# Optimization experiments

Hardware: AMD Instinct MI355X
Metric: run time of the kernel (lower is better)

The kernel has to match this reference:

```python
import jax, jax.numpy as jnp
import numpy as np
import math

B, S, D = 4, 1024, 1024
H, DK = 16, 64
NUM_BUCKETS = 32
MAX_DISTANCE = 128


def _relative_position_bucket(relative_position, bidirectional=True,
                              num_buckets=32, max_distance=128):
    # faithful port of T5's bucketing
    relative_buckets = jnp.zeros_like(relative_position)
    if bidirectional:
        num_buckets //= 2
        relative_buckets = relative_buckets + (relative_position > 0).astype(jnp.int32) * num_buckets
        relative_position = jnp.abs(relative_position)
    else:
        relative_position = -jnp.minimum(relative_position, jnp.zeros_like(relative_position))
    max_exact = num_buckets // 2
    is_small = relative_position < max_exact
    rp_safe = jnp.maximum(relative_position, 1)  # avoid log(0); masked by is_small
    rel_if_large = max_exact + (
        jnp.log(rp_safe.astype(jnp.float32) / max_exact)
        / math.log(max_distance / max_exact) * (num_buckets - max_exact)
    ).astype(jnp.int32)
    rel_if_large = jnp.minimum(rel_if_large, num_buckets - 1)
    return relative_buckets + jnp.where(is_small, relative_position, rel_if_large)


def compute_bias(rel_bias_emb, query_length, key_length):
    ctx = jnp.arange(query_length, dtype=jnp.int32)[:, None]
    mem = jnp.arange(key_length, dtype=jnp.int32)[None, :]
    rp = mem - ctx  # [q, k]
    buckets = _relative_position_bucket(rp, bidirectional=True,
                                        num_buckets=NUM_BUCKETS,
                                        max_distance=MAX_DISTANCE)
    values = rel_bias_emb[buckets]          # [q, k, h]
    return jnp.transpose(values, (2, 0, 1))[None]  # [1, h, q, k]


def setup_inputs() -> dict:
    key = jax.random.key(0)
    ks = jax.random.split(key, 6)
    s = 1.0 / math.sqrt(D)
    return {
        "hidden_states": jax.random.normal(ks[0], (B, S, D), jnp.float32),
        "Wq": jax.random.normal(ks[1], (D, H * DK), jnp.float32) * s,
        "Wk": jax.random.normal(ks[2], (D, H * DK), jnp.float32) * s,
        "Wv": jax.random.normal(ks[3], (D, H * DK), jnp.float32) * s,
        "Wo": jax.random.normal(ks[4], (H * DK, D), jnp.float32) * s,
        "rel_bias_emb": jax.random.normal(ks[5], (NUM_BUCKETS, H), jnp.float32),
    }


def reference(hidden_states, Wq, Wk, Wv, Wo, rel_bias_emb):
    b, s, _ = hidden_states.shape

    def shape_heads(x):  # [b, s, h*dk] -> [b, h, s, dk]
        return x.reshape(b, s, H, DK).transpose(0, 2, 1, 3)

    q = shape_heads(hidden_states @ Wq)
    k = shape_heads(hidden_states @ Wk)
    v = shape_heads(hidden_states @ Wv)

    # T5 attention: no 1/sqrt(dk) scaling
    scores = jnp.einsum('bhqd,bhkd->bhqk', q, k)
    position_bias = compute_bias(rel_bias_emb, s, s)  # [1, h, s, s]
    scores = scores + position_bias
    attn = jax.nn.softmax(scores.astype(jnp.float32), axis=-1).astype(scores.dtype)
    ctx = jnp.einsum('bhqk,bhkd->bhqd', attn, v)
    ctx = ctx.transpose(0, 2, 1, 3).reshape(b, s, H * DK)
    return ctx @ Wo
```

## Files before the change

kernel.cpp:

```cpp
#include <hip/hip_runtime.h>

typedef unsigned short u16;
typedef unsigned int u32;
typedef __bf16 bf16x8 __attribute__((ext_vector_type(8)));
typedef float f32x4 __attribute__((ext_vector_type(4)));

#define MFMA16(a, b, c) __builtin_amdgcn_mfma_f32_16x16x32_bf16(a, b, c, 0, 0, 0)
#define LOG2E 1.4426950408889634f

__device__ __forceinline__ u16 f2bf(float f) {
  u32 u = __float_as_uint(f);
  u += 0x7FFFu + ((u >> 16) & 1u);
  return (u16)(u >> 16);
}

__device__ __forceinline__ void gld16(u16* lds, const u16* g) {
  __builtin_amdgcn_global_load_lds((const __attribute__((address_space(1))) void*)g,
                                   (__attribute__((address_space(3))) void*)lds,
                                   16, 0, 0);
}

__device__ __forceinline__ int t5_bucket(int rp) {
  int ret = rp > 0 ? 16 : 0;
  int a = rp < 0 ? -rp : rp;
  int b;
  if      (a <  8) b = a;
  else if (a < 12) b = 8;
  else if (a < 16) b = 9;
  else if (a < 23) b = 10;
  else if (a < 32) b = 11;
  else if (a < 46) b = 12;
  else if (a < 64) b = 13;
  else if (a < 91) b = 14;
  else             b = 15;
  return ret + b;
}

__global__ __launch_bounds__(256) void prep(const float4* __restrict__ X, ushort4* __restrict__ Xb,
                                            const float* __restrict__ w0, const float* __restrict__ w1,
                                            const float* __restrict__ w2, const float* __restrict__ w3,
                                            u16* __restrict__ out) {
  int bid = blockIdx.x;
  if (bid < 4096) {
    int g = bid * 256 + threadIdx.x;
    float4 v = X[g];
    ushort4 o;
    o.x = f2bf(v.x); o.y = f2bf(v.y); o.z = f2bf(v.z); o.w = f2bf(v.w);
    Xb[g] = o;
    return;
  }
  bid -= 4096;
  const int z = bid >> 8, t = bid & 255;
  const float* W = (z == 0) ? w0 : (z == 1) ? w1 : (z == 2) ? w2 : w3;
  u16* O = out + z * 1048576;
  __shared__ __align__(16) u16 tb[64 * 68];
  const int col = threadIdx.x & 63;
  const int rowo = threadIdx.x >> 6;
  const int n0 = (t & 15) * 64, k0 = (t >> 4) * 64;
#pragma unroll
  for (int r = 0; r < 16; r++) {
    int kl = r * 4 + rowo;
    tb[col * 68 + kl] = f2bf(W[(k0 + kl) * 1024 + n0 + col]);
  }
  __syncthreads();
#pragma unroll
  for (int r = 0; r < 16; r++) {
    int nl = r * 4 + rowo;
    O[(n0 + nl) * 1024 + k0 + col] = tb[nl * 68 + col];
  }
}

__global__ __launch_bounds__(256) void gemm128(const u16* __restrict__ A,
                                               const u16* __restrict__ BtBase,
                                               u16* __restrict__ outp) {
  __shared__ __align__(16) u16 smem[17408];
  u16* sA = smem;
  u16* sB = smem + 8192;
  const int tid = threadIdx.x, lane = tid & 63, wave = tid >> 6;
  const int l15 = lane & 15, quad = lane >> 4;
  const int wm = (wave >> 1) * 64, wn = (wave & 1) * 64;

  const int id = blockIdx.x + blockIdx.y * 24;
  const int xcd = id & 7, jj = id >> 3;
  const int nz = (jj % 12) + (xcd & 1) * 12;
  const int ymb = (jj / 12) + (xcd >> 1) * 8;
  const int n = nz / 3, z = nz % 3;
  const int m0 = ymb * 128, n0 = n * 128;
  const u16* Bt = BtBase + z * 1048576;

  f32x4 acc[4][4];
  const f32x4 vz = {0.f, 0.f, 0.f, 0.f};
#pragma unroll
  for (int i = 0; i < 4; i++)
#pragma unroll
    for (int j = 0; j < 4; j++) acc[i][j] = vz;

  const int sx = l15 & 7;

  for (int kt = 0; kt < 16; kt++) {
    const int ka = kt * 64;
#pragma unroll
    for (int r = 0; r < 4; r++) {
      int cb = r * 256 + wave * 64;
      int cc = cb + lane;
      int row = cc >> 3, c8 = (cc & 7) ^ (row & 7);
      gld16(sA + cb * 8, A  + (m0 + row) * 1024 + ka + c8 * 8);
      gld16(sB + cb * 8, Bt + (n0 + row) * 1024 + ka + c8 * 8);
    }
    __syncthreads();
#pragma unroll
    for (int kk = 0; kk < 2; kk++) {
      bf16x8 af[4], bg[4];
      int g8 = kk * 4 + quad;
#pragma unroll
      for (int mt = 0; mt < 4; mt++)
        af[mt] = *(const bf16x8*)(sA + (wm + mt * 16 + l15) * 64 + (g8 ^ sx) * 8);
#pragma unroll
      for (int nt = 0; nt < 4; nt++)
        bg[nt] = *(const bf16x8*)(sB + (wn + nt * 16 + l15) * 64 + (g8 ^ sx) * 8);
#pragma unroll
      for (int mt = 0; mt < 4; mt++)
#pragma unroll
        for (int nt = 0; nt < 4; nt++)
          acc[mt][nt] = MFMA16(af[mt], bg[nt], acc[mt][nt]);
    }
    __syncthreads();
  }

  if (z == 2) {
    u16* O = outp + z * 4194304;
#pragma unroll
    for (int mt = 0; mt < 4; mt++)
#pragma unroll
      for (int nt = 0; nt < 4; nt++) {
        int col = wn + nt * 16 + l15;
        int rowb = wm + mt * 16 + quad * 4;
        uint2 p;
        p.x = (u32)f2bf(acc[mt][nt][0]) | ((u32)f2bf(acc[mt][nt][1]) << 16);
        p.y = (u32)f2bf(acc[mt][nt][2]) | ((u32)f2bf(acc[mt][nt][3]) << 16);
        *(uint2*)(smem + col * 136 + rowb) = p;
      }
    __syncthreads();
    const int b = m0 >> 10, sbase = m0 & 1023;
#pragma unroll
    for (int p = 0; p < 8; p++) {
      int g = p * 256 + tid;
      int col = g >> 4, chunk = g & 15;
      uint4 v = *(const uint4*)(smem + col * 136 + chunk * 8);
      int nn = n0 + col, hh = nn >> 6, dk = nn & 63;
      *(uint4*)(O + ((b * 16 + hh) * 64 + dk) * 1024 + sbase + chunk * 8) = v;
    }
  } else {
    u16* O = outp + z * 4194304;
    const float scl = (z == 0) ? LOG2E : 1.0f;
#pragma unroll
    for (int mt = 0; mt < 4; mt++)
#pragma unroll
      for (int nt = 0; nt < 4; nt++)
#pragma unroll
        for (int reg = 0; reg < 4; reg++) {
          int row = m0 + wm + mt * 16 + quad * 4 + reg;
          int col = n0 + wn + nt * 16 + l15;
          int bb = row >> 10, s = row & 1023, hh = col >> 6, dk = col & 63;
          O[(bb * 16 + hh) * 65536 + s * 64 + dk] = f2bf(acc[mt][nt][reg] * scl);
        }
  }
}

__global__ __launch_bounds__(256) void attn(const u16* __restrict__ Q, const u16* __restrict__ K,
                                            const u16* __restrict__ V, const float* __restrict__ emb,
                                            u16* __restrict__ ctx) {
  __shared__ __align__(16) u16 sK[64 * 64];
  __shared__ __align__(16) u16 sV[64 * 64];
  __shared__ __align__(16) u16 sP[128 * 72];
  __shared__ __align__(16) float4 bt4[1156];
  const int tid = threadIdx.x, lane = tid & 63, wave = tid >> 6;
  const int l15 = lane & 15, quad = lane >> 4;
  const int bh = blockIdx.x, qt = blockIdx.y;
  const int h = bh & 15, b = bh >> 4;
  const u16* Qp = Q + bh * 65536 + qt * 8192;
  const u16* Kp = K + bh * 65536;
  const u16* Vp = V + bh * 65536;
  const int sx = l15 & 7;

  bf16x8 aq[2][2];
#pragma unroll
  for (int u = 0; u < 2; u++)
#pragma unroll
    for (int kk = 0; kk < 2; kk++)
      aq[u][kk] = *(const bf16x8*)(Qp + (wave * 32 + u * 16 + l15) * 64 + kk * 32 + quad * 8);

  for (int i = tid; i < 1156; i += 256) {
    int rp0 = i - 127 - qt * 128;
    float4 v;
    v.x = emb[t5_bucket(rp0)     * 16 + h] * LOG2E;
    v.y = emb[t5_bucket(rp0 + 1) * 16 + h] * LOG2E;
    v.z = emb[t5_bucket(rp0 + 2) * 16 + h] * LOG2E;
    v.w = emb[t5_bucket(rp0 + 3) * 16 + h] * LOG2E;
    bt4[i] = v;
  }
  const float bias_pos = emb[31 * 16 + h] * LOG2E;
  const float bias_neg = emb[15 * 16 + h] * LOG2E;

  float lsum[2] = {0.f, 0.f};
  f32x4 oc[2][4];
  const f32x4 vzero = {0.f, 0.f, 0.f, 0.f};
#pragma unroll
  for (int u = 0; u < 2; u++)
#pragma unroll
    for (int nt = 0; nt < 4; nt++) oc[u][nt] = vzero;

  __syncthreads();

#pragma unroll 1
  for (int j = 0; j < 16; j++) {
    const u16* Kj = Kp + j * 4096;
#pragma unroll
    for (int r = 0; r < 2; r++) {
      int cb = r * 256 + wave * 64;
      int cc = cb + lane;
      int row = cc >> 3, c8 = (cc & 7) ^ (row & 7);
      gld16(sK + cb * 8, Kj + row * 64 + c8 * 8);
      gld16(sV + cb * 8, Vp + row * 1024 + j * 64 + c8 * 8);
    }
    __syncthreads();

    f32x4 sc[4][2];
    const int rp_min = j * 64 - qt * 128 - 127;
    const int rp_max = j * 64 + 63 - qt * 128;
    if (rp_min >= 91) {
#pragma unroll
      for (int mt = 0; mt < 4; mt++)
#pragma unroll
        for (int u = 0; u < 2; u++) { sc[mt][u][0] = bias_pos; sc[mt][u][1] = bias_pos; sc[mt][u][2] = bias_pos; sc[mt][u][3] = bias_pos; }
    } else if (rp_max <= -91) {
#pragma unroll
      for (int mt = 0; mt < 4; mt++)
#pragma unroll
        for (int u = 0; u < 2; u++) { sc[mt][u][0] = bias_neg; sc[mt][u][1] = bias_neg; sc[mt][u][2] = bias_neg; sc[mt][u][3] = bias_neg; }
    } else {
#pragma unroll
      for (int mt = 0; mt < 4; mt++)
#pragma unroll
        for (int u = 0; u < 2; u++) {
          int idx = j * 64 + mt * 16 + quad * 4 - wave * 32 - u * 16 - l15 + 127;
          float4 bv4 = bt4[idx];
          sc[mt][u][0] = bv4.x; sc[mt][u][1] = bv4.y; sc[mt][u][2] = bv4.z; sc[mt][u][3] = bv4.w;
        }
    }
#pragma unroll
    for (int kk = 0; kk < 2; kk++) {
      bf16x8 ak[4];
      int g8 = kk * 4 + quad;
#pragma unroll
      for (int mt = 0; mt < 4; mt++)
        ak[mt] = *(const bf16x8*)(sK + (mt * 16 + l15) * 64 + (g8 ^ sx) * 8);
#pragma unroll
      for (int mt = 0; mt < 4; mt++)
#pragma unroll
        for (int u = 0; u < 2; u++)
          sc[mt][u] = MFMA16(ak[mt], aq[u][kk], sc[mt][u]);
    }

#pragma unroll
    for (int u = 0; u < 2; u++) {
      const int prow = wave * 32 + u * 16 + l15;
#pragma unroll
      for (int mt = 0; mt < 4; mt++) {
        float p0 = __builtin_amdgcn_exp2f(sc[mt][u][0]);
        float p1 = __builtin_amdgcn_exp2f(sc[mt][u][1]);
        float p2 = __builtin_amdgcn_exp2f(sc[mt][u][2]);
        float p3 = __builtin_amdgcn_exp2f(sc[mt][u][3]);
        lsum[u] += (p0 + p1) + (p2 + p3);
        uint2 pk;
        pk.x = (u32)f2bf(p0) | ((u32)f2bf(p1) << 16);
        pk.y = (u32)f2bf(p2) | ((u32)f2bf(p3) << 16);
        *(uint2*)(sP + prow * 72 + mt * 16 + quad * 4) = pk;
      }
    }
    asm volatile("s_waitcnt lgkmcnt(0)" ::: "memory");

#pragma unroll
    for (int kk = 0; kk < 2; kk++) {
      bf16x8 ap[2];
      int g8 = kk * 4 + quad;
#pragma unroll
      for (int u = 0; u < 2; u++)
        ap[u] = *(const bf16x8*)(sP + (wave * 32 + u * 16 + l15) * 72 + kk * 32 + quad * 8);
#pragma unroll
      for (int nt = 0; nt < 4; nt++) {
        bf16x8 bv = *(const bf16x8*)(sV + (nt * 16 + l15) * 64 + (g8 ^ sx) * 8);
#pragma unroll
        for (int u = 0; u < 2; u++)
          oc[u][nt] = MFMA16(ap[u], bv, oc[u][nt]);
      }
    }
    __syncthreads();
  }

#pragma unroll
  for (int u = 0; u < 2; u++) {
    lsum[u] += __shfl_xor(lsum[u], 16, 64);
    lsum[u] += __shfl_xor(lsum[u], 32, 64);
  }
  float linv[2][4];
#pragma unroll
  for (int u = 0; u < 2; u++)
#pragma unroll
    for (int reg = 0; reg < 4; reg++)
      linv[u][reg] = __builtin_amdgcn_rcpf(__shfl(lsum[u], quad * 4 + reg, 64));

  u16* cb2 = ctx + b * 1048576 + (qt * 128 + wave * 32) * 1024 + h * 64;
#pragma unroll
  for (int u = 0; u < 2; u++)
#pragma unroll
    for (int nt = 0; nt < 4; nt++)
#pragma unroll
      for (int reg = 0; reg < 4; reg++)
        cb2[(u * 16 + quad * 4 + reg) * 1024 + nt * 16 + l15] = f2bf(oc[u][nt][reg] * linv[u][reg]);
}

__global__ __launch_bounds__(256) void gemm_o(const u16* __restrict__ A,
                                              const u16* __restrict__ Bt,
                                              float* __restrict__ O) {
  __shared__ __align__(16) u16 sA[128 * 64];
  __shared__ __align__(16) u16 sB[64 * 64];
  const int tid = threadIdx.x, lane = tid & 63, wave = tid >> 6;
  const int l15 = lane & 15, quad = lane >> 4;
  const int wm = (wave >> 1) * 64, wn = (wave & 1) * 32;
  const int m0 = blockIdx.x * 128, n0 = blockIdx.y * 64;

  f32x4 acc[4][2];
  const f32x4 vz = {0.f, 0.f, 0.f, 0.f};
#pragma unroll
  for (int i = 0; i < 4; i++) { acc[i][0] = vz; acc[i][1] = vz; }

  const int sx = l15 & 7;

  for (int kt = 0; kt < 16; kt++) {
    const int ka = kt * 64;
#pragma unroll
    for (int r = 0; r < 4; r++) {
      int cb = r * 256 + wave * 64;
      int cc = cb + lane;
      int row = cc >> 3, c8 = (cc & 7) ^ (row & 7);
      gld16(sA + cb * 8, A + (m0 + row) * 1024 + ka + c8 * 8);
    }
#pragma unroll
    for (int r = 0; r < 2; r++) {
      int cb = r * 256 + wave * 64;
      int cc = cb + lane;
      int row = cc >> 3, c8 = (cc & 7) ^ (row & 7);
      gld16(sB + cb * 8, Bt + (n0 + row) * 1024 + ka + c8 * 8);
    }
    __syncthreads();
#pragma unroll
    for (int kk = 0; kk < 2; kk++) {
      bf16x8 af[4], bg[2];
      int g8 = kk * 4 + quad;
#pragma unroll
      for (int mt = 0; mt < 4; mt++)
        af[mt] = *(const bf16x8*)(sA + (wm + mt * 16 + l15) * 64 + (g8 ^ sx) * 8);
#pragma unroll
      for (int nt = 0; nt < 2; nt++)
        bg[nt] = *(const bf16x8*)(sB + (wn + nt * 16 + l15) * 64 + (g8 ^ sx) * 8);
#pragma unroll
      for (int mt = 0; mt < 4; mt++)
#pragma unroll
        for (int nt = 0; nt < 2; nt++)
          acc[mt][nt] = MFMA16(af[mt], bg[nt], acc[mt][nt]);
    }
    __syncthreads();
  }

#pragma unroll
  for (int mt = 0; mt < 4; mt++)
#pragma unroll
    for (int nt = 0; nt < 2; nt++)
#pragma unroll
      for (int reg = 0; reg < 4; reg++) {
        int row = m0 + wm + mt * 16 + quad * 4 + reg;
        int col = n0 + wn + nt * 16 + l15;
        O[row * 1024 + col] = acc[mt][nt][reg];
      }
}

extern "C" void kernel_launch(void* const* d_in, const int* in_sizes, int n_in,
                              void* d_out, int out_size, void* d_ws, size_t ws_size,
                              hipStream_t stream) {
  (void)in_sizes; (void)n_in; (void)out_size; (void)ws_size;
  const float* X   = (const float*)d_in[0];
  const float* Wq  = (const float*)d_in[1];
  const float* Wk  = (const float*)d_in[2];
  const float* Wv  = (const float*)d_in[3];
  const float* Wo  = (const float*)d_in[4];
  const float* emb = (const float*)d_in[5];

  char* ws = (char*)d_ws;
  u16* Xb  = (u16*)(ws);
  u16* Wt  = (u16*)(ws + (8u  << 20));
  u16* Qb  = (u16*)(ws + (16u << 20));
  u16* Ctx = (u16*)(ws + (40u << 20));

  prep<<<5120, 256, 0, stream>>>((const float4*)X, (ushort4*)Xb, Wq, Wk, Wv, Wo, Wt);
  gemm128<<<dim3(24, 32), 256, 0, stream>>>(Xb, Wt, Qb);
  attn<<<dim3(64, 8), 256, 0, stream>>>(Qb, Qb + 4194304, Qb + 2 * 4194304, emb, Ctx);
  gemm_o<<<dim3(32, 16), 256, 0, stream>>>(Ctx, Wt + 3 * 1048576, (float*)d_out);
}
```

Measured before the change: 179.5 us.

## Coarsen prep blocks, stage Q/K epilogue through LDS, truncate softmax probabilities

The prep kernel now has each block handle 8 chunks of X conversion or 2 weight-transpose tiles, cutting the grid from 5120 to 1024 blocks. The gemm128 Q/K epilogue now stages results in shared memory and writes 16-byte vectors instead of scattered 2-byte stores, which needs a slightly larger LDS buffer. In attention, exp2 outputs are truncated to bf16 by masking instead of round-to-nearest, and the row sum uses those truncated values split across two accumulators. This saves ALU work but adds a small truncation bias to the probabilities.

```diff
diff --git a/kernel.cpp b/kernel.cpp
--- a/kernel.cpp
+++ b/kernel.cpp
@@ -41,39 +41,47 @@
                                             const float* __restrict__ w2, const float* __restrict__ w3,
                                             u16* __restrict__ out) {
   int bid = blockIdx.x;
-  if (bid < 4096) {
-    int g = bid * 256 + threadIdx.x;
-    float4 v = X[g];
-    ushort4 o;
-    o.x = f2bf(v.x); o.y = f2bf(v.y); o.z = f2bf(v.z); o.w = f2bf(v.w);
-    Xb[g] = o;
+  if (bid < 512) {
+#pragma unroll
+    for (int i = 0; i < 8; i++) {
+      int g = bid * 2048 + i * 256 + threadIdx.x;
+      float4 v = X[g];
+      ushort4 o;
+      o.x = f2bf(v.x); o.y = f2bf(v.y); o.z = f2bf(v.z); o.w = f2bf(v.w);
+      Xb[g] = o;
+    }
     return;
   }
-  bid -= 4096;
-  const int z = bid >> 8, t = bid & 255;
-  const float* W = (z == 0) ? w0 : (z == 1) ? w1 : (z == 2) ? w2 : w3;
-  u16* O = out + z * 1048576;
+  bid -= 512;
   __shared__ __align__(16) u16 tb[64 * 68];
   const int col = threadIdx.x & 63;
   const int rowo = threadIdx.x >> 6;
-  const int n0 = (t & 15) * 64, k0 = (t >> 4) * 64;
-#pragma unroll
-  for (int r = 0; r < 16; r++) {
-    int kl = r * 4 + rowo;
-    tb[col * 68 + kl] = f2bf(W[(k0 + kl) * 1024 + n0 + col]);
-  }
-  __syncthreads();
-#pragma unroll
-  for (int r = 0; r < 16; r++) {
-    int nl = r * 4 + rowo;
-    O[(n0 + nl) * 1024 + k0 + col] = tb[nl * 68 + col];
+#pragma unroll 1
+  for (int t2 = 0; t2 < 2; t2++) {
+    const int tile = bid * 2 + t2;
+    const int z = tile >> 8, t = tile & 255;
+    const float* W = (z == 0) ? w0 : (z == 1) ? w1 : (z == 2) ? w2 : w3;
+    u16* O = out + z * 1048576;
+    const int n0 = (t & 15) * 64, k0 = (t >> 4) * 64;
+#pragma unroll
+    for (int r = 0; r < 16; r++) {
+      int kl = r * 4 + rowo;
+      tb[col * 68 + kl] = f2bf(W[(k0 + kl) * 1024 + n0 + col]);
+    }
+    __syncthreads();
+#pragma unroll
+    for (int r = 0; r < 16; r++) {
+      int nl = r * 4 + rowo;
+      O[(n0 + nl) * 1024 + k0 + col] = tb[nl * 68 + col];
+    }
+    __syncthreads();
   }
 }
 
 __global__ __launch_bounds__(256) void gemm128(const u16* __restrict__ A,
                                                const u16* __restrict__ BtBase,
                                                u16* __restrict__ outp) {
-  __shared__ __align__(16) u16 smem[17408];
+  __shared__ __align__(16) u16 smem[18432];
   u16* sA = smem;
   u16* sB = smem + 8192;
   const int tid = threadIdx.x, lane = tid & 63, wave = tid >> 6;
@@ -156,14 +164,23 @@
 #pragma unroll
     for (int mt = 0; mt < 4; mt++)
 #pragma unroll
-      for (int nt = 0; nt < 4; nt++)
-#pragma unroll
-        for (int reg = 0; reg < 4; reg++) {
-          int row = m0 + wm + mt * 16 + quad * 4 + reg;
-          int col = n0 + wn + nt * 16 + l15;
-          int bb = row >> 10, s = row & 1023, hh = col >> 6, dk = col & 63;
-          O[(bb * 16 + hh) * 65536 + s * 64 + dk] = f2bf(acc[mt][nt][reg] * scl);
-        }
+      for (int nt = 0; nt < 4; nt++) {
+        int rowb = wm + mt * 16 + quad * 4;
+        int colb = wn + nt * 16 + l15;
+#pragma unroll
+        for (int reg = 0; reg < 4; reg++)
+          smem[(rowb + reg) * 144 + colb] = f2bf(acc[mt][nt][reg] * scl);
+      }
+    __syncthreads();
+    const int b = m0 >> 10, sbase = m0 & 1023;
+#pragma unroll
+    for (int p = 0; p < 8; p++) {
+      int g = p * 256 + tid;
+      int ml = g >> 4, c = g & 15;
+      uint4 v = *(const uint4*)(smem + ml * 144 + c * 8);
+      int nn = n0 + c * 8, hh = nn >> 6, dk = nn & 63;
+      *(uint4*)(O + (b * 16 + hh) * 65536 + (sbase + ml) * 64 + dk) = v;
+    }
   }
 }
 
@@ -202,7 +219,7 @@
   const float bias_pos = emb[31 * 16 + h] * LOG2E;
   const float bias_neg = emb[15 * 16 + h] * LOG2E;
 
-  float lsum[2] = {0.f, 0.f};
+  float2 ls2[2] = {{0.f, 0.f}, {0.f, 0.f}};
   f32x4 oc[2][4];
   const f32x4 vzero = {0.f, 0.f, 0.f, 0.f};
 #pragma unroll
@@ -267,14 +284,17 @@
       const int prow = wave * 32 + u * 16 + l15;
 #pragma unroll
       for (int mt = 0; mt < 4; mt++) {
-        float p0 = __builtin_amdgcn_exp2f(sc[mt][u][0]);
-        float p1 = __builtin_amdgcn_exp2f(sc[mt][u][1]);
-        float p2 = __builtin_amdgcn_exp2f(sc[mt][u][2]);
-        float p3 = __builtin_amdgcn_exp2f(sc[mt][u][3]);
-        lsum[u] += (p0 + p1) + (p2 + p3);
+        u32 b0 = __float_as_uint(__builtin_amdgcn_exp2f(sc[mt][u][0]));
+        u32 b1 = __float_as_uint(__builtin_amdgcn_exp2f(sc[mt][u][1]));
+        u32 b2 = __float_as_uint(__builtin_amdgcn_exp2f(sc[mt][u][2]));
+        u32 b3 = __float_as_uint(__builtin_amdgcn_exp2f(sc[mt][u][3]));
+        u32 t0 = b0 & 0xFFFF0000u, t1 = b1 & 0xFFFF0000u;
+        u32 t2 = b2 & 0xFFFF0000u, t3 = b3 & 0xFFFF0000u;
+        ls2[u].x += __uint_as_float(t0) + __uint_as_float(t2);
+        ls2[u].y += __uint_as_float(t1) + __uint_as_float(t3);
         uint2 pk;
-        pk.x = (u32)f2bf(p0) | ((u32)f2bf(p1) << 16);
-        pk.y = (u32)f2bf(p2) | ((u32)f2bf(p3) << 16);
+        pk.x = (t0 >> 16) | t1;
+        pk.y = (t2 >> 16) | t3;
         *(uint2*)(sP + prow * 72 + mt * 16 + quad * 4) = pk;
       }
     }
@@ -298,8 +318,10 @@
     __syncthreads();
   }
 
+  float lsum[2];
 #pragma unroll
   for (int u = 0; u < 2; u++) {
+    lsum[u] = ls2[u].x + ls2[u].y;
     lsum[u] += __shfl_xor(lsum[u], 16, 64);
     lsum[u] += __shfl_xor(lsum[u], 32, 64);
   }
@@ -402,7 +424,7 @@
   u16* Qb  = (u16*)(ws + (16u << 20));
   u16* Ctx = (u16*)(ws + (40u << 20));
 
-  prep<<<5120, 256, 0, stream>>>((const float4*)X, (ushort4*)Xb, Wq, Wk, Wv, Wo, Wt);
+  prep<<<1024, 256, 0, stream>>>((const float4*)X, (ushort4*)Xb, Wq, Wk, Wv, Wo, Wt);
   gemm128<<<dim3(24, 32), 256, 0, stream>>>(Xb, Wt, Qb);
   attn<<<dim3(64, 8), 256, 0, stream>>>(Qb, Qb + 4194304, Qb + 2 * 4194304, emb, Ctx);
   gemm_o<<<dim3(32, 16), 256, 0, stream>>>(Ctx, Wt + 3 * 1048576, (float*)d_out);
```

Result: faster. 173.2 us (-3.5%).
